# Performance work log

Hardware: AMD Instinct MI355X
Metric: run time of the kernel (lower is better)

Reference implementation:

```python
import jax, jax.numpy as jnp
import numpy as np
from jax import lax

B, S, H, E, F, K = 4, 2048, 1024, 8, 4096, 2

def setup_inputs() -> dict:
    key = jax.random.key(0)
    k1, k2, k3, k4 = jax.random.split(key, 4)
    return {
        "hidden_states": jax.random.normal(k1, (B, S, H), dtype=jnp.float32),
        "router_logits": jax.random.normal(k2, (B, S, E), dtype=jnp.float32),
        "w1": jax.random.normal(k3, (E, H, F), dtype=jnp.float32) * 0.02,
        "w2": jax.random.normal(k4, (E, F, H), dtype=jnp.float32) * 0.02,
        "layer_idx": 0,
    }


def reference(hidden_states, router_logits, w1, w2, layer_idx):
    b, s, h = hidden_states.shape
    e = router_logits.shape[-1]
    T = b * s
    x = hidden_states.reshape(T, h)              # [T, H] flattened tokens
    logits = router_logits.reshape(T, e)          # [T, E]

    # top-k routing, softmax over the selected k scores (as in torch.topk + softmax)
    topk_scores, topk_idx = lax.top_k(logits, K)  # [T, K]
    probs = jax.nn.softmax(topk_scores, axis=-1)  # [T, K]

    # scatter combine weights into a dense [T, E] map (dispatch weights)
    cw = jnp.zeros((T, e), dtype=probs.dtype).at[jnp.arange(T)[:, None], topk_idx].add(probs)

    # grouped expert compute: scan over experts, masked weighted accumulation
    def step(acc, ew):
        w1e, w2e, ce = ew                          # [H,F], [F,H], [T]
        he = jax.nn.gelu(x @ w1e) @ w2e            # [T, H] expert FFN
        return acc + ce[:, None] * he, None

    out, _ = lax.scan(step, jnp.zeros_like(x), (w1, w2, cw.T))
    return out.reshape(b, s, h)
```

## Files before the change

kernel.cpp:

```cpp
#include <hip/hip_runtime.h>

#define T_TOKENS 8192
#define H_DIM 1024
#define E_EXP 8
#define F_DIM 4096
#define CAP 8192
#define MT256 16

typedef __attribute__((ext_vector_type(8))) short short8;
typedef __attribute__((ext_vector_type(8))) unsigned short ushort8;
typedef __attribute__((ext_vector_type(4))) float f32x4;

__device__ __forceinline__ unsigned short f2bf(float f) {
    unsigned int u = __float_as_uint(f);
    u += 0x7fffu + ((u >> 16) & 1u);
    return (unsigned short)(u >> 16);
}

__device__ __forceinline__ float gelu_tanh(float x) {
    float z = 0.7978845608028654f * (x + 0.044715f * x * x * x);
    float t = 1.0f - 2.0f / (__expf(2.0f * z) + 1.0f);
    return 0.5f * x * (1.0f + t);
}

__device__ __forceinline__ void gld16(const void* g, void* l) {
    __builtin_amdgcn_global_load_lds(
        (const __attribute__((address_space(1))) unsigned int*)g,
        (__attribute__((address_space(3))) unsigned int*)l,
        16, 0, 0);
}

__global__ void router_kernel(const float* __restrict__ logits,
                              int* __restrict__ cnt,
                              int* __restrict__ tok,
                              float* __restrict__ wt) {
    __shared__ int hcnt[E_EXP];
    __shared__ int hbase[E_EXP];
    int tid = threadIdx.x;
    if (tid < E_EXP) hcnt[tid] = 0;
    __syncthreads();
    int t = blockIdx.x * 256 + tid;
    float l[E_EXP];
#pragma unroll
    for (int i = 0; i < E_EXP; i++) l[i] = logits[t * E_EXP + i];
    int i0 = 0; float s0 = l[0];
#pragma unroll
    for (int i = 1; i < E_EXP; i++) if (l[i] > s0) { s0 = l[i]; i0 = i; }
    int i1 = (i0 == 0) ? 1 : 0; float s1 = l[i1];
#pragma unroll
    for (int i = 0; i < E_EXP; i++) if (i != i0 && l[i] > s1) { s1 = l[i]; i1 = i; }
    float p0 = 1.0f / (1.0f + __expf(s1 - s0));
    float p1 = 1.0f - p0;
    int lo0 = atomicAdd(&hcnt[i0], 1);
    int lo1 = atomicAdd(&hcnt[i1], 1);
    __syncthreads();
    if (tid < E_EXP) hbase[tid] = atomicAdd(&cnt[tid], hcnt[tid]);
    __syncthreads();
    int sl0 = hbase[i0] + lo0;
    tok[i0 * CAP + sl0] = t; wt[i0 * CAP + sl0] = p0;
    int sl1 = hbase[i1] + lo1;
    tok[i1 * CAP + sl1] = t; wt[i1 * CAP + sl1] = p1;
}

__global__ void base_kernel(const int* __restrict__ cnt, int* __restrict__ base) {
    if (threadIdx.x == 0) {
        int b = 0;
        for (int e = 0; e < E_EXP; e++) { base[e] = b; b += cnt[e]; }
    }
}

__global__ void cvtx_kernel(const float* __restrict__ x, unsigned short* __restrict__ xg) {
    int i = blockIdx.x * 256 + threadIdx.x;
    float4 v = ((const float4*)x)[i];
    ushort4 o;
    o.x = f2bf(v.x); o.y = f2bf(v.y); o.z = f2bf(v.z); o.w = f2bf(v.w);
    ((ushort4*)xg)[i] = o;
}

__global__ void tcvt_kernel(const float* __restrict__ in, unsigned short* __restrict__ out,
                            int M, int N) {
    __shared__ float t[64][65];
    size_t eoff = (size_t)blockIdx.z * M * N;
    in += eoff; out += eoff;
    int r0 = blockIdx.x * 64, c0 = blockIdx.y * 64;
    int tid = threadIdx.x;
    int srow = tid >> 4;
    int scol = (tid & 15) * 4;
#pragma unroll
    for (int p = 0; p < 4; p++) {
        int row = p * 16 + srow;
        float4 v = *(const float4*)&in[(size_t)(r0 + row) * N + c0 + scol];
        t[row][scol + 0] = v.x; t[row][scol + 1] = v.y;
        t[row][scol + 2] = v.z; t[row][scol + 3] = v.w;
    }
    __syncthreads();
    int orow = tid >> 3;
    int ocb = (tid & 7) * 8;
#pragma unroll
    for (int p = 0; p < 2; p++) {
        int r = p * 32 + orow;
        ushort8 o;
#pragma unroll
        for (int i = 0; i < 8; i++) o[i] = f2bf(t[ocb + i][r]);
        *(ushort8*)&out[(size_t)(c0 + r) * M + r0 + ocb] = o;
    }
}

template <int GATHER, int EPI, int NT, int KSPLIT>
__global__ __launch_bounds__(512, 2)
void gemm256_kernel(const unsigned short* __restrict__ Asrc,
                    const unsigned short* __restrict__ Bt,
                    int K, int N,
                    const int* __restrict__ cnt, const int* __restrict__ base,
                    const int* __restrict__ tok, const float* __restrict__ wt,
                    unsigned short* __restrict__ Gout, float* __restrict__ out) {
    const int nwg = E_EXP * MT256 * NT * KSPLIT;
    int bid = blockIdx.x;
    int swz = (bid & 7) * (nwg >> 3) + (bid >> 3);
    const int mt = swz & (MT256 - 1);
    int rest = swz >> 4;
    const int ks = rest % KSPLIT; rest /= KSPLIT;
    const int nt = rest % NT;
    const int e  = rest / NT;

    const int cnt_e = cnt[e];
    const int m0 = mt * 256;
    if (m0 >= cnt_e) return;
    const int base_e = base[e];
    const int n0 = nt * 256;
    const int Kp = K / KSPLIT;
    const int kbegin = ks * Kp;
    const int KT = Kp >> 6;

    const int tid = threadIdx.x;
    const int lane = tid & 63;
    const int wave = tid >> 6;
    const int l16 = lane & 15, quad = lane >> 4;
    const int wmg = wave >> 2;
    const int wng = wave & 3;

    __shared__ unsigned short As[2][2][128][64];
    __shared__ unsigned short Bs[2][2][128][64];

    const int rsel = tid >> 3, csel = tid & 7;
    const int swzc = (csel ^ (rsel & 7)) * 8;
    const unsigned short* arow[4];
    const unsigned short* brow[4];
#pragma unroll
    for (int ii = 0; ii < 4; ii++) {
        int gr = m0 + ii * 64 + rsel;
        if (gr > cnt_e - 1) gr = cnt_e - 1;
        const unsigned short* ab;
        if (GATHER) ab = Asrc + (size_t)tok[e * CAP + gr] * K;
        else        ab = Asrc + (size_t)(base_e + gr) * K;
        arow[ii] = ab + kbegin + swzc;
        brow[ii] = Bt + (size_t)e * N * K + (size_t)(n0 + ii * 64 + rsel) * K + kbegin + swzc;
    }
    unsigned short* alds = &As[0][0][0][0];
    unsigned short* blds = &Bs[0][0][0][0];
    const int dstoff = tid * 8;
    const int BUFS = 2 * 128 * 64;

    auto stage = [&](int b, int koff) {
#pragma unroll
        for (int ii = 0; ii < 4; ii++)
            gld16(arow[ii] + koff, alds + b * BUFS + ii * 4096 + dstoff);
#pragma unroll
        for (int ii = 0; ii < 4; ii++)
            gld16(brow[ii] + koff, blds + b * BUFS + ii * 4096 + dstoff);
    };

    f32x4 acc[8][4];
#pragma unroll
    for (int i = 0; i < 8; i++)
#pragma unroll
        for (int j = 0; j < 4; j++) acc[i][j] = (f32x4){0.f, 0.f, 0.f, 0.f};

    const int kx0 = ((quad    ) ^ (l16 & 7)) * 8;
    const int kx1 = ((quad + 4) ^ (l16 & 7)) * 8;

    stage(0, 0);
    int koff = 64;
    for (int t = 0; t < KT; ++t) {
        const int cur = t & 1;
        if (t + 1 < KT) {
            stage(cur ^ 1, koff);
            asm volatile("s_waitcnt vmcnt(8)\n\ts_barrier" ::: "memory");
        } else {
            asm volatile("s_waitcnt vmcnt(0)\n\ts_barrier" ::: "memory");
        }

        short8 bfr[2][4];
#pragma unroll
        for (int j = 0; j < 4; j++) {
            bfr[0][j] = *(const short8*)&Bs[cur][wng >> 1][(wng & 1) * 64 + j * 16 + l16][kx0];
            bfr[1][j] = *(const short8*)&Bs[cur][wng >> 1][(wng & 1) * 64 + j * 16 + l16][kx1];
        }
#pragma unroll
        for (int ms = 0; ms < 2; ms++) {
            short8 afr[2][4];
#pragma unroll
            for (int i = 0; i < 4; i++) {
                afr[0][i] = *(const short8*)&As[cur][wmg][(ms * 4 + i) * 16 + l16][kx0];
                afr[1][i] = *(const short8*)&As[cur][wmg][(ms * 4 + i) * 16 + l16][kx1];
            }
            __builtin_amdgcn_s_setprio(1);
#pragma unroll
            for (int i = 0; i < 4; i++)
#pragma unroll
                for (int j = 0; j < 4; j++) {
                    acc[ms * 4 + i][j] = __builtin_amdgcn_mfma_f32_16x16x32_bf16(
                        afr[0][i], bfr[0][j], acc[ms * 4 + i][j], 0, 0, 0);
                    acc[ms * 4 + i][j] = __builtin_amdgcn_mfma_f32_16x16x32_bf16(
                        afr[1][i], bfr[1][j], acc[ms * 4 + i][j], 0, 0, 0);
                }
            __builtin_amdgcn_s_setprio(0);
        }
        asm volatile("s_barrier" ::: "memory");
        koff += 64;
    }

    if (EPI == 0) {
#pragma unroll
        for (int i = 0; i < 8; i++) {
            int lm = wmg * 128 + i * 16 + quad * 4;
#pragma unroll
            for (int r = 0; r < 4; r++) {
                int gr = m0 + lm + r;
                if (gr < cnt_e) {
                    size_t rowoff = (size_t)(base_e + gr) * N;
#pragma unroll
                    for (int j = 0; j < 4; j++) {
                        int ncol = n0 + wng * 64 + j * 16 + l16;
                        Gout[rowoff + ncol] = f2bf(gelu_tanh(acc[i][j][r]));
                    }
                }
            }
        }
    } else {
#pragma unroll
        for (int i = 0; i < 8; i++) {
            int lm = wmg * 128 + i * 16 + quad * 4;
#pragma unroll
            for (int r = 0; r < 4; r++) {
                int gr = m0 + lm + r;
                if (gr < cnt_e) {
                    int tk = tok[e * CAP + gr];
                    float w = wt[e * CAP + gr];
                    float* orow = out + (size_t)tk * N;
#pragma unroll
                    for (int j = 0; j < 4; j++) {
                        int ncol = n0 + wng * 64 + j * 16 + l16;
                        atomicAdd(&orow[ncol], w * acc[i][j][r]);
                    }
                }
            }
        }
    }
}

extern "C" void kernel_launch(void* const* d_in, const int* in_sizes, int n_in,
                              void* d_out, int out_size, void* d_ws, size_t ws_size,
                              hipStream_t stream) {
    const float* x      = (const float*)d_in[0];
    const float* logits = (const float*)d_in[1];
    const float* w1     = (const float*)d_in[2];
    const float* w2     = (const float*)d_in[3];
    float* out = (float*)d_out;
    char* ws = (char*)d_ws;

    const size_t OFF_CNT  = 0;
    const size_t OFF_BASE = 64;
    const size_t OFF_TOK  = 1024;
    const size_t OFF_WT   = OFF_TOK + (size_t)E_EXP * CAP * 4;
    const size_t OFF_XG   = 1u << 20;
    const size_t OFF_W1T  = OFF_XG + (size_t)T_TOKENS * H_DIM * 2;
    const size_t OFF_W2T  = OFF_W1T + (size_t)E_EXP * H_DIM * F_DIM * 2;
    const size_t OFF_G    = OFF_W2T + (size_t)E_EXP * H_DIM * F_DIM * 2;

    int* cnt  = (int*)(ws + OFF_CNT);
    int* base = (int*)(ws + OFF_BASE);
    int* tok  = (int*)(ws + OFF_TOK);
    float* wt = (float*)(ws + OFF_WT);
    unsigned short* xg  = (unsigned short*)(ws + OFF_XG);
    unsigned short* w1t = (unsigned short*)(ws + OFF_W1T);
    unsigned short* w2t = (unsigned short*)(ws + OFF_W2T);
    unsigned short* G   = (unsigned short*)(ws + OFF_G);

    hipMemsetAsync(d_out, 0, (size_t)out_size * sizeof(float), stream);
    hipMemsetAsync(cnt, 0, 64, stream);

    router_kernel<<<T_TOKENS / 256, 256, 0, stream>>>(logits, cnt, tok, wt);
    base_kernel<<<1, 64, 0, stream>>>(cnt, base);
    cvtx_kernel<<<(T_TOKENS * H_DIM / 4) / 256, 256, 0, stream>>>(x, xg);
    tcvt_kernel<<<dim3(H_DIM / 64, F_DIM / 64, E_EXP), 256, 0, stream>>>(w1, w1t, H_DIM, F_DIM);
    tcvt_kernel<<<dim3(F_DIM / 64, H_DIM / 64, E_EXP), 256, 0, stream>>>(w2, w2t, F_DIM, H_DIM);
    gemm256_kernel<1, 0, 16, 1><<<E_EXP * MT256 * 16 * 1, 512, 0, stream>>>(
        xg, w1t, H_DIM, F_DIM, cnt, base, tok, wt, G, nullptr);
    gemm256_kernel<0, 1, 4, 2><<<E_EXP * MT256 * 4 * 2, 512, 0, stream>>>(
        G, w2t, F_DIM, H_DIM, cnt, base, tok, wt, nullptr, out);
    (void)in_sizes; (void)n_in; (void)ws_size;
}
```

Baseline: 898.0 us.

## Use 4-stage K=32 LDS pipeline and tile-grouped workgroup ordering in expert GEMMs

```diff
diff --git a/kernel.cpp b/kernel.cpp
--- a/kernel.cpp
+++ b/kernel.cpp
@@ -106,7 +106,7 @@
     }
 }
 
-template <int GATHER, int EPI, int NT, int KSPLIT>
+template <int GATHER, int EPI, int NT, int KSPLIT, int NTL, int MTL>
 __global__ __launch_bounds__(512, 2)
 void gemm256_kernel(const unsigned short* __restrict__ Asrc,
                     const unsigned short* __restrict__ Bt,
@@ -116,12 +116,15 @@
                     unsigned short* __restrict__ Gout, float* __restrict__ out) {
     const int nwg = E_EXP * MT256 * NT * KSPLIT;
     int bid = blockIdx.x;
-    int swz = (bid & 7) * (nwg >> 3) + (bid >> 3);
-    const int mt = swz & (MT256 - 1);
-    int rest = swz >> 4;
-    const int ks = rest % KSPLIT; rest /= KSPLIT;
-    const int nt = rest % NT;
-    const int e  = rest / NT;
+    int u = (bid & 7) * (nwg >> 3) + (bid >> 3);
+    const int ntl = u % NTL; u /= NTL;
+    const int mtl = u % MTL; u /= MTL;
+    const int ntb = u % (NT / NTL); u /= (NT / NTL);
+    const int mtb = u % (MT256 / MTL); u /= (MT256 / MTL);
+    const int ks = u % KSPLIT; u /= KSPLIT;
+    const int e = u;
+    const int nt = ntb * NTL + ntl;
+    const int mt = mtb * MTL + mtl;
 
     const int cnt_e = cnt[e];
     const int m0 = mt * 256;
@@ -130,7 +133,7 @@
     const int n0 = nt * 256;
     const int Kp = K / KSPLIT;
     const int kbegin = ks * Kp;
-    const int KT = Kp >> 6;
+    const int KT = Kp >> 5;
 
     const int tid = threadIdx.x;
     const int lane = tid & 63;
@@ -139,35 +142,33 @@
     const int wmg = wave >> 2;
     const int wng = wave & 3;
 
-    __shared__ unsigned short As[2][2][128][64];
-    __shared__ unsigned short Bs[2][2][128][64];
-
-    const int rsel = tid >> 3, csel = tid & 7;
-    const int swzc = (csel ^ (rsel & 7)) * 8;
-    const unsigned short* arow[4];
-    const unsigned short* brow[4];
-#pragma unroll
-    for (int ii = 0; ii < 4; ii++) {
-        int gr = m0 + ii * 64 + rsel;
+    __shared__ unsigned short As[4][256][32];
+    __shared__ unsigned short Bs[4][256][32];
+
+    const int rsel = tid >> 2;
+    const int ksel = (tid & 3) * 8;
+    const unsigned short* arow[2];
+    const unsigned short* brow[2];
+#pragma unroll
+    for (int p = 0; p < 2; p++) {
+        int gr = m0 + p * 128 + rsel;
         if (gr > cnt_e - 1) gr = cnt_e - 1;
         const unsigned short* ab;
         if (GATHER) ab = Asrc + (size_t)tok[e * CAP + gr] * K;
         else        ab = Asrc + (size_t)(base_e + gr) * K;
-        arow[ii] = ab + kbegin + swzc;
-        brow[ii] = Bt + (size_t)e * N * K + (size_t)(n0 + ii * 64 + rsel) * K + kbegin + swzc;
-    }
-    unsigned short* alds = &As[0][0][0][0];
-    unsigned short* blds = &Bs[0][0][0][0];
-    const int dstoff = tid * 8;
-    const int BUFS = 2 * 128 * 64;
+        arow[p] = ab + kbegin + ksel;
+        brow[p] = Bt + (size_t)e * N * K + (size_t)(n0 + p * 128 + rsel) * K + kbegin + ksel;
+    }
+    unsigned short* alds = &As[0][0][0];
+    unsigned short* blds = &Bs[0][0][0];
+    const int dst = tid * 8;
+    const int TSH = 256 * 32;
 
     auto stage = [&](int b, int koff) {
-#pragma unroll
-        for (int ii = 0; ii < 4; ii++)
-            gld16(arow[ii] + koff, alds + b * BUFS + ii * 4096 + dstoff);
-#pragma unroll
-        for (int ii = 0; ii < 4; ii++)
-            gld16(brow[ii] + koff, blds + b * BUFS + ii * 4096 + dstoff);
+        gld16(arow[0] + koff, alds + b * TSH + dst);
+        gld16(arow[1] + koff, alds + b * TSH + 4096 + dst);
+        gld16(brow[0] + koff, blds + b * TSH + dst);
+        gld16(brow[1] + koff, blds + b * TSH + 4096 + dst);
     };
 
     f32x4 acc[8][4];
@@ -176,48 +177,41 @@
 #pragma unroll
         for (int j = 0; j < 4; j++) acc[i][j] = (f32x4){0.f, 0.f, 0.f, 0.f};
 
-    const int kx0 = ((quad    ) ^ (l16 & 7)) * 8;
-    const int kx1 = ((quad + 4) ^ (l16 & 7)) * 8;
-
-    stage(0, 0);
-    int koff = 64;
+    const int kq = quad * 8;
+
+    stage(0, 0); stage(1, 32); stage(2, 64);
+
     for (int t = 0; t < KT; ++t) {
-        const int cur = t & 1;
-        if (t + 1 < KT) {
-            stage(cur ^ 1, koff);
+        const int cur = t & 3;
+        if (t + 3 < KT) {
+            stage((t + 3) & 3, (t + 3) * 32);
+            asm volatile("s_waitcnt vmcnt(12)\n\ts_barrier" ::: "memory");
+        } else if (t + 3 == KT) {
             asm volatile("s_waitcnt vmcnt(8)\n\ts_barrier" ::: "memory");
+        } else if (t + 2 == KT) {
+            asm volatile("s_waitcnt vmcnt(4)\n\ts_barrier" ::: "memory");
         } else {
             asm volatile("s_waitcnt vmcnt(0)\n\ts_barrier" ::: "memory");
         }
 
-        short8 bfr[2][4];
-#pragma unroll
-        for (int j = 0; j < 4; j++) {
-            bfr[0][j] = *(const short8*)&Bs[cur][wng >> 1][(wng & 1) * 64 + j * 16 + l16][kx0];
-            bfr[1][j] = *(const short8*)&Bs[cur][wng >> 1][(wng & 1) * 64 + j * 16 + l16][kx1];
-        }
-#pragma unroll
-        for (int ms = 0; ms < 2; ms++) {
-            short8 afr[2][4];
-#pragma unroll
-            for (int i = 0; i < 4; i++) {
-                afr[0][i] = *(const short8*)&As[cur][wmg][(ms * 4 + i) * 16 + l16][kx0];
-                afr[1][i] = *(const short8*)&As[cur][wmg][(ms * 4 + i) * 16 + l16][kx1];
-            }
-            __builtin_amdgcn_s_setprio(1);
-#pragma unroll
-            for (int i = 0; i < 4; i++)
-#pragma unroll
-                for (int j = 0; j < 4; j++) {
-                    acc[ms * 4 + i][j] = __builtin_amdgcn_mfma_f32_16x16x32_bf16(
-                        afr[0][i], bfr[0][j], acc[ms * 4 + i][j], 0, 0, 0);
-                    acc[ms * 4 + i][j] = __builtin_amdgcn_mfma_f32_16x16x32_bf16(
-                        afr[1][i], bfr[1][j], acc[ms * 4 + i][j], 0, 0, 0);
-                }
-            __builtin_amdgcn_s_setprio(0);
-        }
+        short8 bfr[4];
+#pragma unroll
+        for (int j = 0; j < 4; j++)
+            bfr[j] = *(const short8*)&Bs[cur][wng * 64 + j * 16 + l16][kq];
+        short8 afr[8];
+#pragma unroll
+        for (int i = 0; i < 8; i++)
+            afr[i] = *(const short8*)&As[cur][wmg * 128 + i * 16 + l16][kq];
+
+        __builtin_amdgcn_s_setprio(1);
+#pragma unroll
+        for (int i = 0; i < 8; i++)
+#pragma unroll
+            for (int j = 0; j < 4; j++)
+                acc[i][j] = __builtin_amdgcn_mfma_f32_16x16x32_bf16(afr[i], bfr[j], acc[i][j], 0, 0, 0);
+        __builtin_amdgcn_s_setprio(0);
+
         asm volatile("s_barrier" ::: "memory");
-        koff += 64;
     }
 
     if (EPI == 0) {
@@ -295,9 +289,9 @@
     cvtx_kernel<<<(T_TOKENS * H_DIM / 4) / 256, 256, 0, stream>>>(x, xg);
     tcvt_kernel<<<dim3(H_DIM / 64, F_DIM / 64, E_EXP), 256, 0, stream>>>(w1, w1t, H_DIM, F_DIM);
     tcvt_kernel<<<dim3(F_DIM / 64, H_DIM / 64, E_EXP), 256, 0, stream>>>(w2, w2t, F_DIM, H_DIM);
-    gemm256_kernel<1, 0, 16, 1><<<E_EXP * MT256 * 16 * 1, 512, 0, stream>>>(
+    gemm256_kernel<1, 0, 16, 1, 4, 4><<<E_EXP * MT256 * 16 * 1, 512, 0, stream>>>(
         xg, w1t, H_DIM, F_DIM, cnt, base, tok, wt, G, nullptr);
-    gemm256_kernel<0, 1, 4, 2><<<E_EXP * MT256 * 4 * 2, 512, 0, stream>>>(
+    gemm256_kernel<0, 1, 4, 2, 2, 2><<<E_EXP * MT256 * 4 * 2, 512, 0, stream>>>(
         G, w2t, F_DIM, H_DIM, cnt, base, tok, wt, nullptr, out);
     (void)in_sizes; (void)n_in; (void)ws_size;
 }
```

After: 922.7 us. +2.8%, slower.
